# Optimization experiments

Measured on AMD Instinct MI355X. Metric: run time of the kernel, lower is better.

Reference implementation:

```python
import jax, jax.numpy as jnp
import numpy as np

NUM_HEADS = 8
LN_EPS = 1e-5


def setup_inputs() -> dict:
    key = jax.random.key(0)
    ks = jax.random.split(key, 9)
    B, C, H, W = 8, 512, 32, 32
    s = 1.0 / np.sqrt(C)
    return {
        "f_curr": jax.random.normal(ks[0], (B, C, H, W), dtype=jnp.float32),
        "f_prev": jax.random.normal(ks[1], (B, C, H, W), dtype=jnp.float32),
        "f_next": jax.random.normal(ks[2], (B, C, H, W), dtype=jnp.float32),
        "Wq": jax.random.normal(ks[3], (C, C), dtype=jnp.float32) * s,
        "Wk": jax.random.normal(ks[4], (C, C), dtype=jnp.float32) * s,
        "Wv": jax.random.normal(ks[5], (C, C), dtype=jnp.float32) * s,
        "Wo": jax.random.normal(ks[6], (C, C), dtype=jnp.float32) * s,
        "gamma": jnp.ones((C,), dtype=jnp.float32),
        "beta": jnp.zeros((C,), dtype=jnp.float32),
    }


def _flatten(f):
    # [B,C,H,W] -> [B, H*W, C]
    B, C, H, W = f.shape
    return f.reshape(B, C, H * W).transpose(0, 2, 1)


def reference(f_curr, f_prev, f_next, Wq, Wk, Wv, Wo, gamma, beta):
    B, C, H, W = f_curr.shape
    N = H * W
    hd = C // NUM_HEADS
    scale = hd ** -0.5

    curr_flat = _flatten(f_curr)                              # [B,N,C]
    neigh_flat = jnp.concatenate([_flatten(f_prev), _flatten(f_next)], axis=1)  # [B,2N,C]

    # torch Linear (no bias): y = x @ W.T
    Q = curr_flat @ Wq.T                                      # [B,N,C]
    K = neigh_flat @ Wk.T                                     # [B,2N,C]
    V = neigh_flat @ Wv.T                                     # [B,2N,C]

    def split_heads(t, L):
        return t.reshape(B, L, NUM_HEADS, hd).transpose(0, 2, 1, 3)  # [B,h,L,hd]

    Qh = split_heads(Q, N)
    Kh = split_heads(K, 2 * N)
    Vh = split_heads(V, 2 * N)

    scores = jnp.einsum("bhnd,bhmd->bhnm", Qh, Kh) * scale    # [B,h,N,2N]
    attn = jax.nn.softmax(scores, axis=-1)
    out = jnp.einsum("bhnm,bhmd->bhnd", attn, Vh)             # [B,h,N,hd]

    out = out.transpose(0, 2, 1, 3).reshape(B, N, C)          # merge heads
    out = curr_flat + out @ Wo.T                              # residual

    # LayerNorm over channel dim
    mu = jnp.mean(out, axis=-1, keepdims=True)
    var = jnp.mean(jnp.square(out - mu), axis=-1, keepdims=True)
    out = (out - mu) * jax.lax.rsqrt(var + LN_EPS) * gamma + beta

    return out.transpose(0, 2, 1).reshape(B, C, H, W)
```

## Files before the change

### kernel.cpp

```cpp
#include <hip/hip_runtime.h>
#include <hip/hip_bf16.h>
#include <math.h>

#define NH 8
#define HD 64
#define CH 512
#define NT 1024
#define NB 8

typedef __bf16 bf16_t;
typedef bf16_t bf16x8 __attribute__((ext_vector_type(8)));
typedef bf16_t bf16x4 __attribute__((ext_vector_type(4)));
typedef float  f32x4  __attribute__((ext_vector_type(4)));
typedef float  f32x16 __attribute__((ext_vector_type(16)));
typedef unsigned u32x4 __attribute__((ext_vector_type(4)));

#define MFMA16(a, b, c) __builtin_amdgcn_mfma_f32_16x16x32_bf16((a), (b), (c), 0, 0, 0)
#define MFMA32(a, b, c) __builtin_amdgcn_mfma_f32_32x32x16_bf16((a), (b), (c), 0, 0, 0)
#define EXP2(x) __builtin_amdgcn_exp2f(x)

__device__ __forceinline__ void gload16(const void* g, void* l) {
    __builtin_amdgcn_global_load_lds(
        (const __attribute__((address_space(1))) void*)g,
        (__attribute__((address_space(3))) void*)l, 16, 0, 0);
}

__device__ __forceinline__ unsigned cvtpk(float lo, float hi) {
    unsigned r;
    asm("v_cvt_pk_bf16_f32 %0, %1, %2" : "=v"(r) : "v"(lo), "v"(hi));
    return r;
}

__device__ __forceinline__ void plswap(unsigned& a, unsigned& b) {
    asm("v_permlane32_swap_b32 %0, %1" : "+v"(a), "+v"(b));
}

__global__ __launch_bounds__(256) void prep_kernel(
    const float* __restrict__ fc, const float* __restrict__ fp,
    const float* __restrict__ fn, bf16_t* __restrict__ Xc,
    bf16_t* __restrict__ Xn)
{
    __shared__ __align__(16) bf16_t tile[64 * 64];
    const int t = threadIdx.x;
    const int y = blockIdx.y;
    const int b = y / 3, ft = y % 3;
    const int c0 = (blockIdx.x & 7) * 64;
    const int n0 = (blockIdx.x >> 3) * 64;

    const float* src; bf16_t* dst;
    if (ft == 0)      { src = fc + (size_t)b * CH * NT; dst = Xc + (size_t)b * NT * CH; }
    else if (ft == 1) { src = fp + (size_t)b * CH * NT; dst = Xn + (size_t)b * 2 * NT * CH; }
    else              { src = fn + (size_t)b * CH * NT; dst = Xn + (size_t)b * 2 * NT * CH + (size_t)NT * CH; }

    const int nb = t & 15, cb = t >> 4;
    float4 ld[4];
#pragma unroll
    for (int i = 0; i < 4; ++i)
        ld[i] = *(const float4*)(src + (size_t)(c0 + cb * 4 + i) * NT + n0 + nb * 4);
    const float* lf = (const float*)ld;
#pragma unroll
    for (int j = 0; j < 4; ++j) {
        int n = nb * 4 + j;
        int v = (n >> 2) & 14;
        bf16x4 wv = { (bf16_t)lf[0 * 4 + j], (bf16_t)lf[1 * 4 + j],
                      (bf16_t)lf[2 * 4 + j], (bf16_t)lf[3 * 4 + j] };
        *(bf16x4*)(tile + n * 64 + ((cb ^ v) * 4)) = wv;
    }
    __syncthreads();
#pragma unroll
    for (int i = 0; i < 2; ++i) {
        int gid = t + i * 256;
        int n = gid >> 3, c16 = gid & 7;
        int v = (n >> 2) & 14;
        bf16x8 val = *(const bf16x8*)(tile + n * 64 + (((2 * c16) ^ v) * 4));
        *(bf16x8*)(dst + (size_t)(n0 + n) * CH + c0 + c16 * 8) = val;
    }
}

__global__ __launch_bounds__(256) void wcvt_kernel(
    const float* __restrict__ Wq, const float* __restrict__ Wk,
    const float* __restrict__ Wv, const float* __restrict__ Wo,
    bf16_t* __restrict__ Wb, float* __restrict__ SQz)
{
    const int m = blockIdx.y;
    const float* src = (m == 0) ? Wq : (m == 1) ? Wk : (m == 2) ? Wv : Wo;
    bf16_t* dst = Wb + (size_t)m * CH * CH;
    int gid = blockIdx.x * 256 + threadIdx.x;
    float4 v = *(const float4*)(src + (size_t)gid * 4);
    bf16x4 o = { (bf16_t)v.x, (bf16_t)v.y, (bf16_t)v.z, (bf16_t)v.w };
    *(bf16x4*)(dst + (size_t)gid * 4) = o;
    if (m == 0 && blockIdx.x < 16) {
        f32x4 zz = {0.f, 0.f, 0.f, 0.f};
        *(f32x4*)(SQz + (size_t)(blockIdx.x * 256 + threadIdx.x) * 4) = zz;
    }
}

template <bool SWAP>
__device__ __forceinline__ void gemm_core(const bf16_t* __restrict__ A,
                                          const bf16_t* __restrict__ B,
                                          bf16_t* aT, bf16_t* bT,
                                          f32x4 acc[4][4])
{
    const int t = threadIdx.x, w = t >> 6, lane = t & 63;
    const int lid = lane & 15, quad = lane >> 4;
    const int wm = w >> 1, wn = w & 1;
    const int l4 = lane >> 2, k4 = lane & 3;

    for (int kt = 0; kt < 16; ++kt) {
        const int k0 = kt * 32;
        __syncthreads();
#pragma unroll
        for (int i = 0; i < 2; ++i) {
            int q = w * 2 + i;
            int row = q * 16 + l4;
            int kk = k4 ^ ((row >> 1) & 3);
            gload16(A + (size_t)row * CH + k0 + kk * 8, aT + q * 512);
            gload16(B + (size_t)row * CH + k0 + kk * 8, bT + q * 512);
        }
        __syncthreads();

        const bf16_t* mT = SWAP ? bT : aT;
        const bf16_t* nT = SWAP ? aT : bT;
        bf16x8 mf[4], nf[4];
#pragma unroll
        for (int i = 0; i < 4; ++i) {
            int row = wm * 64 + i * 16 + lid;
            int kw = quad ^ ((row >> 1) & 3);
            mf[i] = *(const bf16x8*)(mT + row * 32 + kw * 8);
        }
#pragma unroll
        for (int i = 0; i < 4; ++i) {
            int row = wn * 64 + i * 16 + lid;
            int kw = quad ^ ((row >> 1) & 3);
            nf[i] = *(const bf16x8*)(nT + row * 32 + kw * 8);
        }
#pragma unroll
        for (int mi = 0; mi < 4; ++mi)
#pragma unroll
            for (int ni = 0; ni < 4; ++ni)
                acc[mi][ni] = MFMA16(mf[mi], nf[ni], acc[mi][ni]);
    }
}

__global__ __launch_bounds__(256) void qkv_kernel(
    const bf16_t* __restrict__ Xc, const bf16_t* __restrict__ Xn,
    const bf16_t* __restrict__ Wb,
    bf16_t* __restrict__ Qn, bf16_t* __restrict__ Kn, bf16_t* __restrict__ Vt)
{
    __shared__ __align__(16) bf16_t aT[128 * 32];
    __shared__ __align__(16) bf16_t bT[128 * 32];
    const int bx = blockIdx.x, b = blockIdx.y;
    const int t = threadIdx.x, w = t >> 6, lane = t & 63;
    const int lid = lane & 15, quad = lane >> 4;
    const int wm = w >> 1, wn = w & 1;
    const float QSC = 0.125f * 1.44269504f;

    f32x4 acc[4][4] = {};

    if (bx < 96) {
        const bf16_t* A; const bf16_t* B; bf16_t* O; float scale;
        if (bx < 32) {
            int nt = bx >> 2, ct = bx & 3;
            A = Xc + (size_t)b * NT * CH + (size_t)nt * 128 * CH;
            B = Wb + (size_t)0 * CH * CH + (size_t)ct * 128 * CH;
            O = Qn + (size_t)b * NT * CH + (size_t)nt * 128 * CH + ct * 128;
            scale = QSC;
        } else {
            int j = bx - 32, nt = j >> 2, ct = j & 3;
            A = Xn + (size_t)b * 2 * NT * CH + (size_t)nt * 128 * CH;
            B = Wb + (size_t)1 * CH * CH + (size_t)ct * 128 * CH;
            O = Kn + (size_t)b * 2 * NT * CH + (size_t)nt * 128 * CH + ct * 128;
            scale = 1.0f;
        }
        gemm_core<false>(A, B, aT, bT, acc);
#pragma unroll
        for (int mi = 0; mi < 4; ++mi)
#pragma unroll
            for (int ni = 0; ni < 4; ++ni)
#pragma unroll
                for (int r = 0; r < 4; ++r) {
                    int n  = wm * 64 + mi * 16 + quad * 4 + r;
                    int co = wn * 64 + ni * 16 + lid;
                    O[(size_t)n * CH + co] = (bf16_t)(acc[mi][ni][r] * scale);
                }
    } else {
        int j = bx - 96, nt = j >> 2, ct = j & 3;
        const bf16_t* A = Xn + (size_t)b * 2 * NT * CH + (size_t)nt * 128 * CH;
        const bf16_t* B = Wb + (size_t)2 * CH * CH + (size_t)ct * 128 * CH;
        bf16_t* O = Vt + (size_t)b * CH * 2 * NT + (size_t)ct * 128 * 2 * NT + nt * 128;
        gemm_core<true>(A, B, aT, bT, acc);
#pragma unroll
        for (int mi = 0; mi < 4; ++mi)
#pragma unroll
            for (int ni = 0; ni < 4; ++ni)
#pragma unroll
                for (int r = 0; r < 4; ++r) {
                    int co_l  = wm * 64 + mi * 16 + quad * 4 + r;
                    int key_l = wn * 64 + ni * 16 + lid;
                    O[(size_t)co_l * (2 * NT) + key_l] = (bf16_t)acc[mi][ni][r];
                }
    }
}

__global__ __launch_bounds__(256, 2) void attn_kernel(
    const bf16_t* __restrict__ Qn, const bf16_t* __restrict__ Kn,
    const bf16_t* __restrict__ Vt, bf16_t* __restrict__ AOn)
{
    __shared__ __align__(16) char smem[65536];
    bf16_t* const kbuf0 = (bf16_t*)smem;
    bf16_t* const kbuf1 = (bf16_t*)(smem + 16384);
    bf16_t* const vbuf0 = (bf16_t*)(smem + 32768);
    bf16_t* const vbuf1 = (bf16_t*)(smem + 49152);
    float*  const scr_all = (float*)smem;
    bf16_t* const obuf    = (bf16_t*)(smem + 36864);
    float*  const l_scr   = (float*)(smem + 55296);

    const int t = threadIdx.x;
    const int w = t >> 6, lane = t & 63;
    const int wq = w >> 1, wk = w & 1;
    const int l31 = lane & 31, h = lane >> 5;

    const int bid = blockIdx.x;
    const int xcd = bid & 7, ii = bid >> 3;
    const int grp = xcd * 8 + (ii >> 3);
    const int qt  = ii & 7;
    const int b = grp >> 3, hh = grp & 7;
    const int q0 = qt * 128;

    const bf16_t* Qb  = Qn + ((size_t)b * NT + q0) * CH + hh * HD;
    const bf16_t* Kb  = Kn + (size_t)b * 2 * NT * CH + hh * HD;
    const bf16_t* Vtb = Vt + ((size_t)b * CH + hh * HD) * (2 * NT);
    bf16_t* AOb = AOn + ((size_t)b * NT + q0) * CH + hh * HD;

#define STAGE_KV(kbn, kw, vw)                                                  \
    {                                                                          \
        _Pragma("unroll")                                                      \
        for (int i = 0; i < 4; ++i) {                                          \
            int ck = w * 64 + i * 256 + lane;                                  \
            int kr = ck >> 3, kg = ck & 7;                                     \
            gload16(Kb + (size_t)((kbn) + kr) * CH + ((kg ^ (kr & 7)) * 8),    \
                    (kw) + (w * 64 + i * 256) * 8);                            \
            int cv = ck;                                                       \
            int vr = cv >> 4, vg = cv & 15;                                    \
            gload16(Vtb + (size_t)vr * (2 * NT) + (kbn) + ((vg ^ (vr & 15)) * 8), \
                    (vw) + (w * 64 + i * 256) * 8);                            \
        }                                                                      \
    }

    const bf16_t* Qrow = Qb + (size_t)(wq * 64 + l31) * CH + h * 8;
    bf16x8 qf[2][4];
#pragma unroll
    for (int nf = 0; nf < 2; ++nf)
#pragma unroll
        for (int ks = 0; ks < 4; ++ks)
            qf[nf][ks] = *(const bf16x8*)(Qrow + (size_t)nf * 32 * CH + ks * 16);

    STAGE_KV(0, kbuf0, vbuf0);
    __syncthreads();

    f32x16 o[2][2] = {};
    float lpart[2] = {0.f, 0.f};

    const int swk = l31 & 7;
    const int swv = l31 & 15;

    for (int kt = 0; kt < 16; ++kt) {
        const int cur = kt & 1;
        const bf16_t* const kr_buf = cur ? kbuf1 : kbuf0;
        const bf16_t* const vr_buf = cur ? vbuf1 : vbuf0;
        bf16_t* const kw_buf = cur ? kbuf0 : kbuf1;
        bf16_t* const vw_buf = cur ? vbuf0 : vbuf1;

        if (kt < 15)
            STAGE_KV((kt + 1) * 128, kw_buf, vw_buf);

#pragma unroll
        for (int mf = 0; mf < 2; ++mf) {
            const int krow = wk * 64 + mf * 32 + l31;
            bf16x8 kfm[4];
#pragma unroll
            for (int ks = 0; ks < 4; ++ks)
                kfm[ks] = *(const bf16x8*)(kr_buf + krow * 64 + (((ks * 2 + h) ^ swk) * 8));

            f32x16 s[2] = {};
            __builtin_amdgcn_s_setprio(1);
#pragma unroll
            for (int ks = 0; ks < 4; ++ks)
#pragma unroll
                for (int nf = 0; nf < 2; ++nf)
                    s[nf] = MFMA32(kfm[ks], qf[nf][ks], s[nf]);
            __builtin_amdgcn_s_setprio(0);

            bf16x8 pfrag[2][2];
#pragma unroll
            for (int nf = 0; nf < 2; ++nf) {
                float p[16];
#pragma unroll
                for (int r = 0; r < 16; ++r) p[r] = EXP2(s[nf][r]);
                lpart[nf] += ((p[0] + p[1]) + (p[2] + p[3]))
                           + ((p[4] + p[5]) + (p[6] + p[7]))
                           + ((p[8] + p[9]) + (p[10] + p[11]))
                           + ((p[12] + p[13]) + (p[14] + p[15]));
                unsigned a0 = cvtpk(p[0], p[1]),   b0 = cvtpk(p[4], p[5]);
                unsigned a1 = cvtpk(p[2], p[3]),   b1 = cvtpk(p[6], p[7]);
                unsigned a2 = cvtpk(p[8], p[9]),   b2 = cvtpk(p[12], p[13]);
                unsigned a3 = cvtpk(p[10], p[11]), b3 = cvtpk(p[14], p[15]);
                plswap(a0, b0); plswap(a1, b1); plswap(a2, b2); plswap(a3, b3);
                u32x4 f0 = { a0, a1, b0, b1 };
                u32x4 f1 = { a2, a3, b2, b3 };
                pfrag[nf][0] = __builtin_bit_cast(bf16x8, f0);
                pfrag[nf][1] = __builtin_bit_cast(bf16x8, f1);
            }

            __builtin_amdgcn_s_setprio(1);
#pragma unroll
            for (int fi = 0; fi < 2; ++fi) {
                const int ks = mf * 2 + fi;
                bf16x8 av[2];
#pragma unroll
                for (int df = 0; df < 2; ++df) {
                    int vrow = df * 32 + l31;
                    av[df] = *(const bf16x8*)(vr_buf + vrow * 128 +
                             (((wk * 8 + ks * 2 + h) ^ swv) * 8));
                }
#pragma unroll
                for (int df = 0; df < 2; ++df)
#pragma unroll
                    for (int nf = 0; nf < 2; ++nf)
                        o[df][nf] = MFMA32(av[df], pfrag[nf][fi], o[df][nf]);
            }
            __builtin_amdgcn_s_setprio(0);
        }
        __syncthreads();
    }
#undef STAGE_KV

    float l2[2];
#pragma unroll
    for (int nf = 0; nf < 2; ++nf)
        l2[nf] = lpart[nf] + __shfl_xor(lpart[nf], 32);

    if (wk == 1) {
        float* scr = scr_all + wq * 4352;
#pragma unroll
        for (int df = 0; df < 2; ++df)
#pragma unroll
            for (int nf = 0; nf < 2; ++nf) {
                int qrow = nf * 32 + l31;
#pragma unroll
                for (int g = 0; g < 4; ++g) {
                    int d = df * 32 + 8 * g + 4 * h;
                    f32x4 v = { o[df][nf][4 * g + 0], o[df][nf][4 * g + 1],
                                o[df][nf][4 * g + 2], o[df][nf][4 * g + 3] };
                    *(f32x4*)(scr + qrow * 68 + d) = v;
                }
            }
        if (h == 0) {
            l_scr[wq * 64 + 0 * 32 + l31] = l2[0];
            l_scr[wq * 64 + 1 * 32 + l31] = l2[1];
        }
    }
    __syncthreads();

    if (wk == 0) {
        const float* scr = scr_all + wq * 4352;
        float inv[2];
#pragma unroll
        for (int nf = 0; nf < 2; ++nf)
            inv[nf] = 1.0f / (l2[nf] + l_scr[wq * 64 + nf * 32 + l31]);
#pragma unroll
        for (int df = 0; df < 2; ++df)
#pragma unroll
            for (int nf = 0; nf < 2; ++nf) {
                int qrow = nf * 32 + l31;
#pragma unroll
                for (int g = 0; g < 4; ++g) {
                    int d = df * 32 + 8 * g + 4 * h;
                    f32x4 part = *(const f32x4*)(scr + qrow * 68 + d);
                    bf16x4 ov = {
                        (bf16_t)((o[df][nf][4 * g + 0] + part.x) * inv[nf]),
                        (bf16_t)((o[df][nf][4 * g + 1] + part.y) * inv[nf]),
                        (bf16_t)((o[df][nf][4 * g + 2] + part.z) * inv[nf]),
                        (bf16_t)((o[df][nf][4 * g + 3] + part.w) * inv[nf]) };
                    int qg = wq * 64 + qrow;
                    *(bf16x4*)(obuf + qg * 72 + (d ^ (qg & 24))) = ov;
                }
            }
    }
    __syncthreads();

#pragma unroll
    for (int i = 0; i < 4; ++i) {
        int gid = t + i * 256;
        int qr = gid >> 3, c8 = (gid & 7) * 8;
        *(bf16x8*)(AOb + (size_t)qr * CH + c8) =
            *(const bf16x8*)(obuf + qr * 72 + (c8 ^ (qr & 24)));
    }
}

__global__ __launch_bounds__(256) void proj_kernel(
    const bf16_t* __restrict__ AOn, const bf16_t* __restrict__ Wb,
    const float* __restrict__ fc, float* __restrict__ Zt,
    float* __restrict__ Ssum, float* __restrict__ Ssq)
{
    __shared__ __align__(16) bf16_t aT[128 * 32];
    __shared__ __align__(16) bf16_t bT[128 * 32];
    const int bx = blockIdx.x, b = blockIdx.y;
    const int nt = bx >> 2, ct = bx & 3;
    const int t = threadIdx.x, w = t >> 6, lane = t & 63;
    const int lid = lane & 15, quad = lane >> 4;
    const int wm = w >> 1, wn = w & 1;

    const bf16_t* A = AOn + (size_t)b * NT * CH + (size_t)nt * 128 * CH;
    const bf16_t* B = Wb + (size_t)3 * CH * CH + (size_t)ct * 128 * CH;

    f32x4 acc[4][4] = {};
    gemm_core<true>(A, B, aT, bT, acc);

    const size_t bofs = (size_t)b * CH * NT;
    float sP[4] = {0.f, 0.f, 0.f, 0.f}, qP[4] = {0.f, 0.f, 0.f, 0.f};
#pragma unroll
    for (int mi = 0; mi < 4; ++mi)
#pragma unroll
        for (int ni = 0; ni < 4; ++ni)
#pragma unroll
            for (int r = 0; r < 4; ++r) {
                int co_l = wm * 64 + mi * 16 + quad * 4 + r;
                int n_l  = wn * 64 + ni * 16 + lid;
                size_t idx = bofs + (size_t)(ct * 128 + co_l) * NT + nt * 128 + n_l;
                float z = acc[mi][ni][r] + fc[idx];
                Zt[idx] = z;
                sP[ni] += z;
                qP[ni] += z * z;
            }
#pragma unroll
    for (int ni = 0; ni < 4; ++ni) {
        sP[ni] += __shfl_xor(sP[ni], 16);  sP[ni] += __shfl_xor(sP[ni], 32);
        qP[ni] += __shfl_xor(qP[ni], 16);  qP[ni] += __shfl_xor(qP[ni], 32);
    }
    __syncthreads();
    float* sRed = (float*)aT;
    float* qRed = sRed + 256;
    if (quad == 0) {
#pragma unroll
        for (int ni = 0; ni < 4; ++ni) {
            sRed[w * 64 + ni * 16 + lid] = sP[ni];
            qRed[w * 64 + ni * 16 + lid] = qP[ni];
        }
    }
    __syncthreads();
    if (t < 128) {
        float s = sRed[t] + sRed[128 + t];
        float q = qRed[t] + qRed[128 + t];
        atomicAdd(&Ssum[(size_t)b * NT + nt * 128 + t], s);
        atomicAdd(&Ssq [(size_t)b * NT + nt * 128 + t], q);
    }
}

__global__ __launch_bounds__(256) void apply_kernel(
    const float* __restrict__ Zt, const float* __restrict__ Ssum,
    const float* __restrict__ Ssq, const float* __restrict__ gamma,
    const float* __restrict__ beta, float* __restrict__ out)
{
    const int row = blockIdx.x;
    const int co = row & 511, b = row >> 9;
    const int t = threadIdx.x;
    const float g = gamma[co], be = beta[co];
    const size_t base = (size_t)row * NT + t * 4;
    f32x4 z  = *(const f32x4*)(Zt + base);
    f32x4 S  = *(const f32x4*)(Ssum + (size_t)b * NT + t * 4);
    f32x4 Q2 = *(const f32x4*)(Ssq  + (size_t)b * NT + t * 4);
    f32x4 o;
#pragma unroll
    for (int c = 0; c < 4; ++c) {
        float mu  = S[c] * (1.0f / 512.0f);
        float var = Q2[c] * (1.0f / 512.0f) - mu * mu;
        float rs  = rsqrtf(var + 1e-5f);
        o[c] = (z[c] - mu) * rs * g + be;
    }
    *(f32x4*)(out + base) = o;
}

extern "C" void kernel_launch(void* const* d_in, const int* in_sizes, int n_in,
                              void* d_out, int out_size, void* d_ws, size_t ws_size,
                              hipStream_t stream)
{
    (void)in_sizes; (void)n_in; (void)out_size; (void)ws_size;
    const float* fc    = (const float*)d_in[0];
    const float* fp    = (const float*)d_in[1];
    const float* fn    = (const float*)d_in[2];
    const float* Wq    = (const float*)d_in[3];
    const float* Wk    = (const float*)d_in[4];
    const float* Wv    = (const float*)d_in[5];
    const float* Wo    = (const float*)d_in[6];
    const float* gamma = (const float*)d_in[7];
    const float* beta  = (const float*)d_in[8];
    float* out = (float*)d_out;

    char* ws = (char*)d_ws;
    bf16_t* Xn  = (bf16_t*)(ws);
    bf16_t* Qn  = (bf16_t*)(ws + 16777216);
    bf16_t* Kn  = (bf16_t*)(ws + 25165824);
    bf16_t* Xc  = (bf16_t*)(ws + 41943040);
    bf16_t* AOn = Xc;
    bf16_t* Vt  = (bf16_t*)(ws + 50331648);
    bf16_t* Wb  = (bf16_t*)(ws + 67108864);
    float*  Ssum = (float*)(ws + 69206016);
    float*  Ssq  = (float*)(ws + 69238784);
    float*  Zt  = (float*)(ws);

    prep_kernel<<<dim3(128, 24), 256, 0, stream>>>(fc, fp, fn, Xc, Xn);
    wcvt_kernel<<<dim3(256, 4), 256, 0, stream>>>(Wq, Wk, Wv, Wo, Wb, Ssum);
    qkv_kernel<<<dim3(160, 8), 256, 0, stream>>>(Xc, Xn, Wb, Qn, Kn, Vt);
    attn_kernel<<<dim3(512), 256, 0, stream>>>(Qn, Kn, Vt, AOn);
    proj_kernel<<<dim3(32, 8), 256, 0, stream>>>(AOn, Wb, fc, Zt, Ssum, Ssq);
    apply_kernel<<<4096, 256, 0, stream>>>(Zt, Ssum, Ssq, gamma, beta, out);
}
```

Baseline: 208.0 us.

## Double-buffer LDS tiles in shared GEMM core and raise MFMA wave priority

Result: no change. 207.5 us (-0.3%).

```diff
diff --git a/kernel.cpp b/kernel.cpp
--- a/kernel.cpp
+++ b/kernel.cpp
@@ -98,7 +98,8 @@
 template <bool SWAP>
 __device__ __forceinline__ void gemm_core(const bf16_t* __restrict__ A,
                                           const bf16_t* __restrict__ B,
-                                          bf16_t* aT, bf16_t* bT,
+                                          bf16_t* aT0, bf16_t* bT0,
+                                          bf16_t* aT1, bf16_t* bT1,
                                           f32x4 acc[4][4])
 {
     const int t = threadIdx.x, w = t >> 6, lane = t & 63;
@@ -106,21 +107,33 @@
     const int wm = w >> 1, wn = w & 1;
     const int l4 = lane >> 2, k4 = lane & 3;
 
+#define GSTAGE(k0, aT, bT)                                                     \
+    {                                                                          \
+        _Pragma("unroll")                                                      \
+        for (int i = 0; i < 2; ++i) {                                          \
+            int q = w * 2 + i;                                 \
+            int row = q * 16 + l4;                                             \
+            int kk = k4 ^ ((row >> 1) & 3);                                    \
+            gload16(A + (size_t)row * CH + (k0) + kk * 8, (aT) + q * 512);     \
+            gload16(B + (size_t)row * CH + (k0) + kk * 8, (bT) + q * 512);     \
+        }                                                                      \
+    }
+
+    GSTAGE(0, aT0, bT0);
+    __syncthreads();
+
     for (int kt = 0; kt < 16; ++kt) {
-        const int k0 = kt * 32;
-        __syncthreads();
-#pragma unroll
-        for (int i = 0; i < 2; ++i) {
-            int q = w * 2 + i;
-            int row = q * 16 + l4;
-            int kk = k4 ^ ((row >> 1) & 3);
-            gload16(A + (size_t)row * CH + k0 + kk * 8, aT + q * 512);
-            gload16(B + (size_t)row * CH + k0 + kk * 8, bT + q * 512);
-        }
-        __syncthreads();
-
-        const bf16_t* mT = SWAP ? bT : aT;
-        const bf16_t* nT = SWAP ? aT : bT;
+        const int cur = kt & 1;
+        const bf16_t* aTr = cur ? aT1 : aT0;
+        const bf16_t* bTr = cur ? bT1 : bT0;
+        if (kt < 15) {
+            bf16_t* aTw = cur ? aT0 : aT1;
+            bf16_t* bTw = cur ? bT0 : bT1;
+            GSTAGE((kt + 1) * 32, aTw, bTw);
+        }
+
+        const bf16_t* mT = SWAP ? bTr : aTr;
+        const bf16_t* nT = SWAP ? aTr : bTr;
         bf16x8 mf[4], nf[4];
 #pragma unroll
         for (int i = 0; i < 4; ++i) {
@@ -134,12 +147,16 @@
             int kw = quad ^ ((row >> 1) & 3);
             nf[i] = *(const bf16x8*)(nT + row * 32 + kw * 8);
         }
+        __builtin_amdgcn_s_setprio(1);
 #pragma unroll
         for (int mi = 0; mi < 4; ++mi)
 #pragma unroll
             for (int ni = 0; ni < 4; ++ni)
                 acc[mi][ni] = MFMA16(mf[mi], nf[ni], acc[mi][ni]);
-    }
+        __builtin_amdgcn_s_setprio(0);
+        __syncthreads();
+    }
+#undef GSTAGE
 }
 
 __global__ __launch_bounds__(256) void qkv_kernel(
@@ -147,8 +164,10 @@
     const bf16_t* __restrict__ Wb,
     bf16_t* __restrict__ Qn, bf16_t* __restrict__ Kn, bf16_t* __restrict__ Vt)
 {
-    __shared__ __align__(16) bf16_t aT[128 * 32];
-    __shared__ __align__(16) bf16_t bT[128 * 32];
+    __shared__ __align__(16) bf16_t aT0[128 * 32];
+    __shared__ __align__(16) bf16_t bT0[128 * 32];
+    __shared__ __align__(16) bf16_t aT1[128 * 32];
+    __shared__ __align__(16) bf16_t bT1[128 * 32];
     const int bx = blockIdx.x, b = blockIdx.y;
     const int t = threadIdx.x, w = t >> 6, lane = t & 63;
     const int lid = lane & 15, quad = lane >> 4;
@@ -172,7 +191,7 @@
             O = Kn + (size_t)b * 2 * NT * CH + (size_t)nt * 128 * CH + ct * 128;
             scale = 1.0f;
         }
-        gemm_core<false>(A, B, aT, bT, acc);
+        gemm_core<false>(A, B, aT0, bT0, aT1, bT1, acc);
 #pragma unroll
         for (int mi = 0; mi < 4; ++mi)
 #pragma unroll
@@ -188,7 +207,7 @@
         const bf16_t* A = Xn + (size_t)b * 2 * NT * CH + (size_t)nt * 128 * CH;
         const bf16_t* B = Wb + (size_t)2 * CH * CH + (size_t)ct * 128 * CH;
         bf16_t* O = Vt + (size_t)b * CH * 2 * NT + (size_t)ct * 128 * 2 * NT + nt * 128;
-        gemm_core<true>(A, B, aT, bT, acc);
+        gemm_core<true>(A, B, aT0, bT0, aT1, bT1, acc);
 #pragma unroll
         for (int mi = 0; mi < 4; ++mi)
 #pragma unroll
@@ -403,8 +422,10 @@
     const float* __restrict__ fc, float* __restrict__ Zt,
     float* __restrict__ Ssum, float* __restrict__ Ssq)
 {
-    __shared__ __align__(16) bf16_t aT[128 * 32];
-    __shared__ __align__(16) bf16_t bT[128 * 32];
+    __shared__ __align__(16) bf16_t aT0[128 * 32];
+    __shared__ __align__(16) bf16_t bT0[128 * 32];
+    __shared__ __align__(16) bf16_t aT1[128 * 32];
+    __shared__ __align__(16) bf16_t bT1[128 * 32];
     const int bx = blockIdx.x, b = blockIdx.y;
     const int nt = bx >> 2, ct = bx & 3;
     const int t = threadIdx.x, w = t >> 6, lane = t & 63;
@@ -415,7 +436,7 @@
     const bf16_t* B = Wb + (size_t)3 * CH * CH + (size_t)ct * 128 * CH;
 
     f32x4 acc[4][4] = {};
-    gemm_core<true>(A, B, aT, bT, acc);
+    gemm_core<true>(A, B, aT0, bT0, aT1, bT1, acc);
 
     const size_t bofs = (size_t)b * CH * NT;
     float sP[4] = {0.f, 0.f, 0.f, 0.f}, qP[4] = {0.f, 0.f, 0.f, 0.f};
@@ -439,7 +460,7 @@
         qP[ni] += __shfl_xor(qP[ni], 16);  qP[ni] += __shfl_xor(qP[ni], 32);
     }
     __syncthreads();
-    float* sRed = (float*)aT;
+    float* sRed = (float*)aT0;
     float* qRed = sRed + 256;
     if (quad == 0) {
 #pragma unroll
```
